# Kernel optimization log

Measured on AMD Instinct MI355X. Metric: run time of the kernel, lower is better.

The kernel has to match this reference:

```python
import jax, jax.numpy as jnp
import numpy as np
import math

D_MODEL = 1024
NUM_HEADS = 16
D_K = D_MODEL // NUM_HEADS


def setup_inputs() -> dict:
    key = jax.random.key(0)
    ks = jax.random.split(key, 9)
    s = 1.0 / math.sqrt(D_MODEL)
    x = jax.random.normal(ks[0], (2, 2048, D_MODEL), dtype=jnp.float32)
    # torch Linear params: weight [out, in], bias [out]
    Wq = jax.random.uniform(ks[1], (D_MODEL, D_MODEL), jnp.float32, -s, s)
    bq = jax.random.uniform(ks[2], (D_MODEL,), jnp.float32, -s, s)
    Wk = jax.random.uniform(ks[3], (D_MODEL, D_MODEL), jnp.float32, -s, s)
    bk = jax.random.uniform(ks[4], (D_MODEL,), jnp.float32, -s, s)
    Wv = jax.random.uniform(ks[5], (D_MODEL, D_MODEL), jnp.float32, -s, s)
    bv = jax.random.uniform(ks[6], (D_MODEL,), jnp.float32, -s, s)
    Wo = jax.random.uniform(ks[7], (D_MODEL, D_MODEL), jnp.float32, -s, s)
    bo = jax.random.uniform(ks[8], (D_MODEL,), jnp.float32, -s, s)
    return {"x": x, "Wq": Wq, "bq": bq, "Wk": Wk, "bk": bk,
            "Wv": Wv, "bv": bv, "Wo": Wo, "bo": bo}


def reference(x, Wq, bq, Wk, bk, Wv, bv, Wo, bo):
    B, T, _ = x.shape
    scale = 1.0 / math.sqrt(D_MODEL)  # NOTE: module scales by sqrt(d_model), not sqrt(d_k)

    def proj(W, b):
        # torch Linear: x @ W^T + b, then split heads -> [B, H, T, d_k]
        y = jnp.einsum('btd,ed->bte', x, W) + b
        return y.reshape(B, T, NUM_HEADS, D_K).transpose(0, 2, 1, 3)

    Q = proj(Wq, bq)
    K = proj(Wk, bk)
    V = proj(Wv, bv)
    logits = jnp.einsum('bhtd,bhsd->bhts', Q, K) * scale  # [B,H,T,T]
    attn = jax.nn.softmax(logits, axis=-1)
    out = jnp.einsum('bhts,bhsd->bhtd', attn, V)  # [B,H,T,d_k]
    out = out.transpose(0, 2, 1, 3).reshape(B, T, D_MODEL)
    return jnp.einsum('btd,ed->bte', out, Wo) + bo
```

## Files before the change

### kernel.cpp

```cpp
#include <hip/hip_runtime.h>

#define T_SEQ 2048
#define NB 2
#define NH 16
#define DK 64
#define DMODEL 1024

typedef __bf16 bf16x8 __attribute__((ext_vector_type(8)));
typedef float f32x4 __attribute__((ext_vector_type(4)));
typedef unsigned short ushortx8 __attribute__((ext_vector_type(8)));
typedef unsigned short ushortx4 __attribute__((ext_vector_type(4)));

__device__ inline unsigned short f2b1(float f) {
  unsigned u = __float_as_uint(f);
  u += 0x7fffu + ((u >> 16) & 1u);
  return (unsigned short)(u >> 16);
}

__device__ inline void gload16(const void* g, void* l) {
  __builtin_amdgcn_global_load_lds((const __attribute__((address_space(1))) void*)g,
                                   (__attribute__((address_space(3))) void*)l, 16, 0, 0);
}

__global__ void prep(const float* __restrict__ x,
                     const float* __restrict__ w0, const float* __restrict__ w1,
                     const float* __restrict__ w2, const float* __restrict__ w3,
                     const float* __restrict__ bq, const float* __restrict__ bk,
                     const float* __restrict__ bv,
                     unsigned short* __restrict__ xb, unsigned short* __restrict__ Wqkv,
                     float* __restrict__ bqkv) {
  int bid = blockIdx.x, tid = threadIdx.x;
  if (bid < 4096) {
    int i = (bid * 256 + tid) * 4;
    float4 v = *(const float4*)(x + i);
    ushortx4 o;
    o.x = f2b1(v.x); o.y = f2b1(v.y); o.z = f2b1(v.z); o.w = f2b1(v.w);
    *(ushortx4*)(xb + i) = o;
  } else if (bid < 8192) {
    int which = (bid - 4096) >> 10;
    int i = (((bid - 4096) & 1023) * 256 + tid) * 4;
    const float* src = which == 0 ? w0 : which == 1 ? w1 : which == 2 ? w2 : w3;
    float4 v = *(const float4*)(src + i);
    ushortx4 o;
    o.x = f2b1(v.x); o.y = f2b1(v.y); o.z = f2b1(v.z); o.w = f2b1(v.w);
    *(ushortx4*)(Wqkv + (long)which * 1048576 + i) = o;
  } else {
    int i = (bid - 8192) * 256 + tid;
    if (i < 3072) {
      float v = (i < 1024) ? bq[i] : (i < 2048 ? bk[i - 1024] : bv[i - 2048]);
      bqkv[i] = v;
    }
  }
}

__global__ __launch_bounds__(256, 2)
void gemm_bt(const unsigned short* __restrict__ A, const unsigned short* __restrict__ B,
             const float* __restrict__ bias, unsigned short* __restrict__ Cb,
             float* __restrict__ Cf, int M, int N, int K, int scale_cols, float scl) {
  __shared__ unsigned short As[2][4096];
  __shared__ unsigned short Bs[2][4096];
  const int tid = threadIdx.x;
  const int w = tid >> 6, lane = tid & 63;
  const int quad = lane >> 4, l16 = lane & 15;
  const int bm = blockIdx.y, bn = blockIdx.x;
  const int wm = w >> 1, wn = w & 1;

  f32x4 acc[4][4] = {};

  const int srow = tid >> 2;
  const int c4 = tid & 3;
  const unsigned short* aG = A + (long)(bm * 128 + srow) * K + c4 * 8;
  const unsigned short* bG = B + (long)(bn * 128 + srow) * K + c4 * 8;
  const long rs64 = (long)64 * K;
  const int wo = w * 512;

  gload16(aG, As[0] + wo);
  gload16(aG + rs64, As[0] + 2048 + wo);
  gload16(bG, Bs[0] + wo);
  gload16(bG + rs64, Bs[0] + 2048 + wo);

  int buf = 0;
  for (int kt = 0; kt < K; kt += 32) {
    __syncthreads();
    {
      const int nb = buf ^ 1;
      gload16(aG + kt + 32, As[nb] + wo);
      gload16(aG + rs64 + kt + 32, As[nb] + 2048 + wo);
      gload16(bG + kt + 32, Bs[nb] + wo);
      gload16(bG + rs64 + kt + 32, Bs[nb] + 2048 + wo);
    }

    bf16x8 af[4], bfr[4];
#pragma unroll
    for (int mt = 0; mt < 4; mt++)
      af[mt] = *(const bf16x8*)(As[buf] + (wm * 64 + mt * 16 + l16) * 32 + quad * 8);
#pragma unroll
    for (int nt = 0; nt < 4; nt++)
      bfr[nt] = *(const bf16x8*)(Bs[buf] + (wn * 64 + nt * 16 + l16) * 32 + quad * 8);
#pragma unroll
    for (int mt = 0; mt < 4; mt++)
#pragma unroll
      for (int nt = 0; nt < 4; nt++)
        acc[mt][nt] = __builtin_amdgcn_mfma_f32_16x16x32_bf16(af[mt], bfr[nt], acc[mt][nt], 0, 0, 0);
    buf ^= 1;
  }

  const int col0 = bn * 128 + wn * 64 + l16;
#pragma unroll
  for (int mt = 0; mt < 4; mt++) {
    int row0 = bm * 128 + wm * 64 + mt * 16 + quad * 4;
#pragma unroll
    for (int nt = 0; nt < 4; nt++) {
      int col = col0 + nt * 16;
      float bb = bias[col];
      float s = (col < scale_cols) ? scl : 1.0f;
#pragma unroll
      for (int r = 0; r < 4; r++) {
        float v = (acc[mt][nt][r] + bb) * s;
        if (Cf) Cf[(long)(row0 + r) * N + col] = v;
        else    Cb[(long)(row0 + r) * N + col] = f2b1(v);
      }
    }
  }
}

__global__ __launch_bounds__(256)
void vtrans(const unsigned short* __restrict__ QKV, unsigned short* __restrict__ Vt) {
  __shared__ unsigned short tile[64 * 80];
  int tid = threadIdx.x;
  int b = blockIdx.y >> 4, h = blockIdx.y & 15, tt = blockIdx.x;
  const unsigned short* base = QKV + (long)(b * T_SEQ + tt * 64) * 3072 + 2048 + h * 64;
#pragma unroll
  for (int rr = 0; rr < 2; rr++) {
    int L = rr * 256 + tid;
    int row = L >> 3, c = L & 7;
    ushortx8 v = *(const ushortx8*)(base + (long)row * 3072 + c * 8);
    *(ushortx8*)(tile + row * 80 + c * 8) = v;
  }
  __syncthreads();
  unsigned short* obase = Vt + (long)((b * NH + h) * DK) * T_SEQ + tt * 64;
#pragma unroll
  for (int rr = 0; rr < 2; rr++) {
    int L = rr * 256 + tid;
    int d = L >> 3, c = L & 7;
    ushortx8 o;
#pragma unroll
    for (int j = 0; j < 8; j++) o[j] = tile[(c * 8 + j) * 80 + d];
    *(ushortx8*)(obase + (long)d * T_SEQ + c * 8) = o;
  }
}

__global__ __launch_bounds__(256)
void attn2(const unsigned short* __restrict__ QKV, const unsigned short* __restrict__ Vt,
           float* __restrict__ Onum, float* __restrict__ Oden) {
  __shared__ unsigned short Ks[2][4096];
  __shared__ unsigned short Vs[2][4096];
  __shared__ unsigned short Ps[4 * 1152];
  const int tid = threadIdx.x;
  const int w = tid >> 6, lane = tid & 63;
  const int quad = lane >> 4, l16 = lane & 15;

  const int id = blockIdx.x;
  const int group = (id & 7) | (((id >> 3) & 7) << 3);
  const int qt = id >> 6;
  const int bh = group >> 1, split = group & 1;
  const int b = bh >> 4, h = bh & 15;
  const long qkvBase = (long)b * T_SEQ * 3072;
  const int kv0 = split * 1024;

  bf16x8 qf[2][2];
#pragma unroll
  for (int g = 0; g < 2; g++) {
    const unsigned short* qp = QKV + qkvBase + (long)(qt * 128 + w * 32 + g * 16 + l16) * 3072 + h * 64 + quad * 8;
    qf[g][0] = *(const bf16x8*)qp;
    qf[g][1] = *(const bf16x8*)(qp + 32);
  }

  const unsigned short* kG[2];
  const unsigned short* vG[2];
#pragma unroll
  for (int i = 0; i < 2; i++) {
    int S = w * 128 + i * 64 + lane;
    int krow = S >> 3;
    int kc = (S & 7) ^ ((krow >> 2) & 7);
    kG[i] = QKV + qkvBase + 1024 + h * 64 + (long)(kv0 + krow) * 3072 + kc * 8;
    int vc = (S & 7) ^ (krow & 7);
    vG[i] = Vt + (long)bh * DK * T_SEQ + (long)krow * T_SEQ + kv0 + vc * 8;
  }
  unsigned short* psW = Ps + w * 1152;
  const int wo2 = w * 1024;

  gload16(kG[0], Ks[0] + wo2);
  gload16(kG[1], Ks[0] + wo2 + 512);
  gload16(vG[0], Vs[0] + wo2);
  gload16(vG[1], Vs[0] + wo2 + 512);
  kG[0] += 64 * 3072; kG[1] += 64 * 3072;
  vG[0] += 64;        vG[1] += 64;

  f32x4 acco[2][4] = {};
  float psum[2][4] = {};
  int buf = 0;

  for (int it = 0; it < 16; it++) {
    __syncthreads();
    {
      const int nb = buf ^ 1;
      gload16(kG[0], Ks[nb] + wo2);
      gload16(kG[1], Ks[nb] + wo2 + 512);
      gload16(vG[0], Vs[nb] + wo2);
      gload16(vG[1], Vs[nb] + wo2 + 512);
      kG[0] += 64 * 3072; kG[1] += 64 * 3072;
      vG[0] += 64;        vG[1] += 64;
    }

    const int sw = (l16 & 7) * 16;
    f32x4 s[2][4];
#pragma unroll
    for (int nt = 0; nt < 4; nt++) {
      const char* kb = (char*)(Ks[buf]) + (4 * l16 + nt) * 128;
      bf16x8 k0 = *(const bf16x8*)(kb + ((quad * 16) ^ sw));
      bf16x8 k1 = *(const bf16x8*)(kb + ((64 + quad * 16) ^ sw));
#pragma unroll
      for (int g = 0; g < 2; g++) {
        f32x4 z = {};
        z = __builtin_amdgcn_mfma_f32_16x16x32_bf16(qf[g][0], k0, z, 0, 0, 0);
        z = __builtin_amdgcn_mfma_f32_16x16x32_bf16(qf[g][1], k1, z, 0, 0, 0);
        s[g][nt] = z;
      }
    }

    bf16x8 pa[2][2];
#pragma unroll
    for (int g = 0; g < 2; g++) {
#pragma unroll
      for (int r = 0; r < 4; r++) {
        float p0 = __builtin_amdgcn_exp2f(s[g][0][r]);
        float p1 = __builtin_amdgcn_exp2f(s[g][1][r]);
        float p2 = __builtin_amdgcn_exp2f(s[g][2][r]);
        float p3 = __builtin_amdgcn_exp2f(s[g][3][r]);
        psum[g][r] += (p0 + p1) + (p2 + p3);
        unsigned a0 = __float_as_uint(p0) + 0x8000u;
        unsigned a1 = __float_as_uint(p1) + 0x8000u;
        unsigned a2 = __float_as_uint(p2) + 0x8000u;
        unsigned a3 = __float_as_uint(p3) + 0x8000u;
        uint2 pk;
        pk.x = __builtin_amdgcn_perm(a1, a0, 0x07060302u);
        pk.y = __builtin_amdgcn_perm(a3, a2, 0x07060302u);
        *(uint2*)(psW + (quad * 4 + r) * 72 + l16 * 4) = pk;
      }
      pa[g][0] = *(const bf16x8*)(psW + l16 * 72 + quad * 8);
      pa[g][1] = *(const bf16x8*)(psW + l16 * 72 + 32 + quad * 8);
    }

#pragma unroll
    for (int nt = 0; nt < 4; nt++) {
      const char* vb = (char*)(Vs[buf]) + (nt * 16 + l16) * 128;
      bf16x8 v0 = *(const bf16x8*)(vb + ((quad * 16) ^ sw));
      bf16x8 v1 = *(const bf16x8*)(vb + ((64 + quad * 16) ^ sw));
#pragma unroll
      for (int g = 0; g < 2; g++) {
        acco[g][nt] = __builtin_amdgcn_mfma_f32_16x16x32_bf16(pa[g][0], v0, acco[g][nt], 0, 0, 0);
        acco[g][nt] = __builtin_amdgcn_mfma_f32_16x16x32_bf16(pa[g][1], v1, acco[g][nt], 0, 0, 0);
      }
    }
    buf ^= 1;
  }

  const long rowBase = (long)bh * T_SEQ + qt * 128 + w * 32;
  const long numBase = ((long)split * 65536 + rowBase) * 64;
#pragma unroll
  for (int g = 0; g < 2; g++)
#pragma unroll
    for (int r = 0; r < 4; r++) {
      float v = psum[g][r];
      v += __shfl_xor(v, 1, 64);
      v += __shfl_xor(v, 2, 64);
      v += __shfl_xor(v, 4, 64);
      v += __shfl_xor(v, 8, 64);
      if (l16 == 0)
        Oden[(long)split * 65536 + rowBase + g * 16 + quad * 4 + r] = v;
#pragma unroll
      for (int nt = 0; nt < 4; nt++)
        Onum[numBase + (long)(g * 16 + quad * 4 + r) * 64 + nt * 16 + l16] = acco[g][nt][r];
    }
}

__global__ __launch_bounds__(256)
void combine(const float* __restrict__ Onum, const float* __restrict__ Oden,
             unsigned short* __restrict__ Ob) {
  int idx = blockIdx.x * 256 + threadIdx.x;
  int rp = idx >> 4;
  int dq = (idx & 15) * 4;
  float4 n0 = *(const float4*)(Onum + (long)rp * 64 + dq);
  float4 n1 = *(const float4*)(Onum + 4194304L + (long)rp * 64 + dq);
  float den = Oden[rp] + Oden[65536 + rp];
  float rl = __builtin_amdgcn_rcpf(den);
  int bh = rp >> 11, t = rp & 2047;
  int b = bh >> 4, h = bh & 15;
  ushortx4 o;
  o.x = f2b1((n0.x + n1.x) * rl);
  o.y = f2b1((n0.y + n1.y) * rl);
  o.z = f2b1((n0.z + n1.z) * rl);
  o.w = f2b1((n0.w + n1.w) * rl);
  *(ushortx4*)(Ob + (long)(b * T_SEQ + t) * DMODEL + h * 64 + dq) = o;
}

extern "C" void kernel_launch(void* const* d_in, const int* in_sizes, int n_in,
                              void* d_out, int out_size, void* d_ws, size_t ws_size,
                              hipStream_t stream) {
  const float* x  = (const float*)d_in[0];
  const float* Wq = (const float*)d_in[1];
  const float* bq = (const float*)d_in[2];
  const float* Wk = (const float*)d_in[3];
  const float* bk = (const float*)d_in[4];
  const float* Wv = (const float*)d_in[5];
  const float* bv = (const float*)d_in[6];
  const float* Wo = (const float*)d_in[7];
  const float* bo = (const float*)d_in[8];
  float* out = (float*)d_out;

  unsigned short* xb   = (unsigned short*)d_ws;
  unsigned short* Wqkv = xb + 4194304;
  unsigned short* Wob  = Wqkv + 3145728;
  float*          bqkv = (float*)(Wob + 1048576);
  unsigned short* QKV  = (unsigned short*)(bqkv + 3072);
  unsigned short* Vt   = QKV + 12582912;
  unsigned short* Ob   = Vt + 4194304;
  float*          Onum = (float*)(Ob + 4194304);
  float*          Oden = Onum + 8388608;

  prep<<<8204, 256, 0, stream>>>(x, Wq, Wk, Wv, Wo, bq, bk, bv, xb, Wqkv, bqkv);

  gemm_bt<<<dim3(24, 32), 256, 0, stream>>>(xb, Wqkv, bqkv, QKV, nullptr,
                                            4096, 3072, 1024, 1024, 0.04508422037f);

  vtrans<<<dim3(32, 32), 256, 0, stream>>>(QKV, Vt);
  attn2<<<dim3(1024), 256, 0, stream>>>(QKV, Vt, Onum, Oden);
  combine<<<dim3(4096), 256, 0, stream>>>(Onum, Oden, Ob);

  gemm_bt<<<dim3(8, 32), 256, 0, stream>>>(Ob, Wob, bo, nullptr, out,
                                           4096, 1024, 1024, 0, 1.0f);
}
```

Before: 215.5 us.

## Compute transposed scores to keep P in registers, dropping LDS round-trip

The attention kernel now computes S^T = K·Q^T by swapping the MFMA operands, so each lane's score accumulators line up directly with the A-operand layout of the P·V MFMA. This lets the bf16 probabilities be packed in registers instead of written to and read back from a shared-memory P buffer. The V fragments are reassembled from two 8-byte LDS reads to match the permuted k ordering. The K swizzle is simplified, the row-sum reduction uses cross-quad shuffles, and launch bounds now request 4 blocks per CU, which risks register spills.

```diff
diff --git a/kernel.cpp b/kernel.cpp
--- a/kernel.cpp
+++ b/kernel.cpp
@@ -20,6 +20,11 @@
 __device__ inline void gload16(const void* g, void* l) {
   __builtin_amdgcn_global_load_lds((const __attribute__((address_space(1))) void*)g,
                                    (__attribute__((address_space(3))) void*)l, 16, 0, 0);
+}
+
+__device__ inline bf16x8 mk8(unsigned a, unsigned b, unsigned c, unsigned d) {
+  uint4 t = {a, b, c, d};
+  return *(bf16x8*)&t;
 }
 
 __global__ void prep(const float* __restrict__ x,
@@ -150,12 +155,11 @@
   }
 }
 
-__global__ __launch_bounds__(256)
-void attn2(const unsigned short* __restrict__ QKV, const unsigned short* __restrict__ Vt,
+__global__ __launch_bounds__(256, 4)
+void attn3(const unsigned short* __restrict__ QKV, const unsigned short* __restrict__ Vt,
            float* __restrict__ Onum, float* __restrict__ Oden) {
   __shared__ unsigned short Ks[2][4096];
   __shared__ unsigned short Vs[2][4096];
-  __shared__ unsigned short Ps[4 * 1152];
   const int tid = threadIdx.x;
   const int w = tid >> 6, lane = tid & 63;
   const int quad = lane >> 4, l16 = lane & 15;
@@ -181,13 +185,11 @@
 #pragma unroll
   for (int i = 0; i < 2; i++) {
     int S = w * 128 + i * 64 + lane;
-    int krow = S >> 3;
-    int kc = (S & 7) ^ ((krow >> 2) & 7);
-    kG[i] = QKV + qkvBase + 1024 + h * 64 + (long)(kv0 + krow) * 3072 + kc * 8;
-    int vc = (S & 7) ^ (krow & 7);
-    vG[i] = Vt + (long)bh * DK * T_SEQ + (long)krow * T_SEQ + kv0 + vc * 8;
-  }
-  unsigned short* psW = Ps + w * 1152;
+    int row = S >> 3;
+    int c = (S & 7) ^ (row & 7);
+    kG[i] = QKV + qkvBase + 1024 + h * 64 + (long)(kv0 + row) * 3072 + c * 8;
+    vG[i] = Vt + (long)bh * DK * T_SEQ + (long)row * T_SEQ + kv0 + c * 8;
+  }
   const int wo2 = w * 1024;
 
   gload16(kG[0], Ks[0] + wo2);
@@ -198,8 +200,9 @@
   vG[0] += 64;        vG[1] += 64;
 
   f32x4 acco[2][4] = {};
-  float psum[2][4] = {};
+  float psum[2] = {0.f, 0.f};
   int buf = 0;
+  const int e16 = (l16 & 7) * 16;
 
   for (int it = 0; it < 16; it++) {
     __syncthreads();
@@ -213,54 +216,56 @@
       vG[0] += 64;        vG[1] += 64;
     }
 
-    const int sw = (l16 & 7) * 16;
-    f32x4 s[2][4];
+    f32x4 st[2][4];
 #pragma unroll
     for (int nt = 0; nt < 4; nt++) {
-      const char* kb = (char*)(Ks[buf]) + (4 * l16 + nt) * 128;
-      bf16x8 k0 = *(const bf16x8*)(kb + ((quad * 16) ^ sw));
-      bf16x8 k1 = *(const bf16x8*)(kb + ((64 + quad * 16) ^ sw));
+      const char* kr = (char*)(Ks[buf]) + (nt * 16 + l16) * 128;
+      bf16x8 k0 = *(const bf16x8*)(kr + ((quad * 16) ^ e16));
+      bf16x8 k1 = *(const bf16x8*)(kr + (((quad + 4) * 16) ^ e16));
 #pragma unroll
       for (int g = 0; g < 2; g++) {
         f32x4 z = {};
-        z = __builtin_amdgcn_mfma_f32_16x16x32_bf16(qf[g][0], k0, z, 0, 0, 0);
-        z = __builtin_amdgcn_mfma_f32_16x16x32_bf16(qf[g][1], k1, z, 0, 0, 0);
-        s[g][nt] = z;
+        z = __builtin_amdgcn_mfma_f32_16x16x32_bf16(k0, qf[g][0], z, 0, 0, 0);
+        z = __builtin_amdgcn_mfma_f32_16x16x32_bf16(k1, qf[g][1], z, 0, 0, 0);
+        st[g][nt] = z;
       }
     }
 
     bf16x8 pa[2][2];
 #pragma unroll
     for (int g = 0; g < 2; g++) {
-#pragma unroll
-      for (int r = 0; r < 4; r++) {
-        float p0 = __builtin_amdgcn_exp2f(s[g][0][r]);
-        float p1 = __builtin_amdgcn_exp2f(s[g][1][r]);
-        float p2 = __builtin_amdgcn_exp2f(s[g][2][r]);
-        float p3 = __builtin_amdgcn_exp2f(s[g][3][r]);
-        psum[g][r] += (p0 + p1) + (p2 + p3);
+      unsigned pk[4][2];
+#pragma unroll
+      for (int nt = 0; nt < 4; nt++) {
+        float p0 = __builtin_amdgcn_exp2f(st[g][nt][0]);
+        float p1 = __builtin_amdgcn_exp2f(st[g][nt][1]);
+        float p2 = __builtin_amdgcn_exp2f(st[g][nt][2]);
+        float p3 = __builtin_amdgcn_exp2f(st[g][nt][3]);
+        psum[g] += (p0 + p1) + (p2 + p3);
         unsigned a0 = __float_as_uint(p0) + 0x8000u;
         unsigned a1 = __float_as_uint(p1) + 0x8000u;
         unsigned a2 = __float_as_uint(p2) + 0x8000u;
         unsigned a3 = __float_as_uint(p3) + 0x8000u;
-        uint2 pk;
-        pk.x = __builtin_amdgcn_perm(a1, a0, 0x07060302u);
-        pk.y = __builtin_amdgcn_perm(a3, a2, 0x07060302u);
-        *(uint2*)(psW + (quad * 4 + r) * 72 + l16 * 4) = pk;
+        pk[nt][0] = __builtin_amdgcn_perm(a1, a0, 0x07060302u);
+        pk[nt][1] = __builtin_amdgcn_perm(a3, a2, 0x07060302u);
       }
-      pa[g][0] = *(const bf16x8*)(psW + l16 * 72 + quad * 8);
-      pa[g][1] = *(const bf16x8*)(psW + l16 * 72 + 32 + quad * 8);
-    }
-
+      pa[g][0] = mk8(pk[0][0], pk[0][1], pk[1][0], pk[1][1]);
+      pa[g][1] = mk8(pk[2][0], pk[2][1], pk[3][0], pk[3][1]);
+    }
+
+    const int off8 = (quad & 1) * 8;
+    const int cq = quad >> 1;
 #pragma unroll
     for (int nt = 0; nt < 4; nt++) {
-      const char* vb = (char*)(Vs[buf]) + (nt * 16 + l16) * 128;
-      bf16x8 v0 = *(const bf16x8*)(vb + ((quad * 16) ^ sw));
-      bf16x8 v1 = *(const bf16x8*)(vb + ((64 + quad * 16) ^ sw));
-#pragma unroll
-      for (int g = 0; g < 2; g++) {
-        acco[g][nt] = __builtin_amdgcn_mfma_f32_16x16x32_bf16(pa[g][0], v0, acco[g][nt], 0, 0, 0);
-        acco[g][nt] = __builtin_amdgcn_mfma_f32_16x16x32_bf16(pa[g][1], v1, acco[g][nt], 0, 0, 0);
+      const char* vr = (char*)(Vs[buf]) + (nt * 16 + l16) * 128;
+#pragma unroll
+      for (int km = 0; km < 2; km++) {
+        uint2 lo = *(const uint2*)(vr + (((km * 4 + cq) * 16) ^ e16) + off8);
+        uint2 hi = *(const uint2*)(vr + (((km * 4 + cq + 2) * 16) ^ e16) + off8);
+        bf16x8 vf = mk8(lo.x, lo.y, hi.x, hi.y);
+#pragma unroll
+        for (int g = 0; g < 2; g++)
+          acco[g][nt] = __builtin_amdgcn_mfma_f32_16x16x32_bf16(pa[g][km], vf, acco[g][nt], 0, 0, 0);
       }
     }
     buf ^= 1;
@@ -269,20 +274,18 @@
   const long rowBase = (long)bh * T_SEQ + qt * 128 + w * 32;
   const long numBase = ((long)split * 65536 + rowBase) * 64;
 #pragma unroll
-  for (int g = 0; g < 2; g++)
-#pragma unroll
-    for (int r = 0; r < 4; r++) {
-      float v = psum[g][r];
-      v += __shfl_xor(v, 1, 64);
-      v += __shfl_xor(v, 2, 64);
-      v += __shfl_xor(v, 4, 64);
-      v += __shfl_xor(v, 8, 64);
-      if (l16 == 0)
-        Oden[(long)split * 65536 + rowBase + g * 16 + quad * 4 + r] = v;
-#pragma unroll
-      for (int nt = 0; nt < 4; nt++)
+  for (int g = 0; g < 2; g++) {
+    float v = psum[g];
+    v += __shfl_xor(v, 16, 64);
+    v += __shfl_xor(v, 32, 64);
+    if (lane < 16)
+      Oden[(long)split * 65536 + rowBase + g * 16 + lane] = v;
+#pragma unroll
+    for (int nt = 0; nt < 4; nt++)
+#pragma unroll
+      for (int r = 0; r < 4; r++)
         Onum[numBase + (long)(g * 16 + quad * 4 + r) * 64 + nt * 16 + l16] = acco[g][nt][r];
-    }
+  }
 }
 
 __global__ __launch_bounds__(256)
@@ -335,7 +338,7 @@
                                             4096, 3072, 1024, 1024, 0.04508422037f);
 
   vtrans<<<dim3(32, 32), 256, 0, stream>>>(QKV, Vt);
-  attn2<<<dim3(1024), 256, 0, stream>>>(QKV, Vt, Onum, Oden);
+  attn3<<<dim3(1024), 256, 0, stream>>>(QKV, Vt, Onum, Oden);
   combine<<<dim3(4096), 256, 0, stream>>>(Onum, Oden, Ob);
 
   gemm_bt<<<dim3(8, 32), 256, 0, stream>>>(Ob, Wob, bo, nullptr, out,
```

Result: faster. 206.5 us (-4.2%).
